# Performance work log

Measured on AMD Instinct MI355X. Metric: run time of the kernel, lower is better.

## Reference

```python
import jax, jax.numpy as jnp
import numpy as np

HIDDEN = 2048
N_HEADS = 16
N_KV_GROUPS = 4
HEAD_DIM = HIDDEN // N_HEADS  # 128
LATENT = 512
KV_SIZE = HIDDEN * N_KV_GROUPS // N_HEADS  # 512


def setup_inputs() -> dict:
    key = jax.random.key(0)
    ks = jax.random.split(key, 11)
    s = 0.02
    return {
        "hidden_states": jax.random.normal(ks[0], (2, 2048, HIDDEN), dtype=jnp.float32),
        "Wq": jax.random.normal(ks[1], (HIDDEN, HIDDEN), dtype=jnp.float32) * s,
        "bq": jnp.zeros((HIDDEN,), dtype=jnp.float32),
        "Wl": jax.random.normal(ks[2], (HIDDEN, LATENT), dtype=jnp.float32) * s,
        "bl": jnp.zeros((LATENT,), dtype=jnp.float32),
        "Wk": jax.random.normal(ks[3], (LATENT, KV_SIZE), dtype=jnp.float32) * s,
        "bk": jnp.zeros((KV_SIZE,), dtype=jnp.float32),
        "Wv": jax.random.normal(ks[4], (LATENT, KV_SIZE), dtype=jnp.float32) * s,
        "bv": jnp.zeros((KV_SIZE,), dtype=jnp.float32),
        "Wo": jax.random.normal(ks[5], (HIDDEN, HIDDEN), dtype=jnp.float32) * s,
        "bo": jnp.zeros((HIDDEN,), dtype=jnp.float32),
    }


def reference(hidden_states, Wq, bq, Wl, bl, Wk, bk, Wv, bv, Wo, bo):
    B, S, _ = hidden_states.shape
    heads_per_group = N_HEADS // N_KV_GROUPS

    q = hidden_states @ Wq + bq                      # [B,S,H*D]
    latent = hidden_states @ Wl + bl                 # [B,S,L]
    k = latent @ Wk + bk                             # [B,S,G*D]
    v = latent @ Wv + bv

    q = q.reshape(B, S, N_HEADS, HEAD_DIM).transpose(0, 2, 1, 3)        # [B,H,S,D]
    k = k.reshape(B, S, N_KV_GROUPS, HEAD_DIM).transpose(0, 2, 1, 3)    # [B,G,S,D]
    v = v.reshape(B, S, N_KV_GROUPS, HEAD_DIM).transpose(0, 2, 1, 3)

    # repeat_interleave over head dim: group g -> heads [g*hpg, (g+1)*hpg)
    k = jnp.repeat(k, heads_per_group, axis=1)       # [B,H,S,D]
    v = jnp.repeat(v, heads_per_group, axis=1)

    scale = 1.0 / np.sqrt(HEAD_DIM).astype(np.float32)
    scores = jnp.einsum("bhqd,bhkd->bhqk", q, k) * scale
    probs = jax.nn.softmax(scores, axis=-1)          # dropout p=0 (eval) -> identity
    ctx = jnp.einsum("bhqk,bhkd->bhqd", probs, v)    # [B,H,S,D]
    ctx = ctx.transpose(0, 2, 1, 3).reshape(B, S, HIDDEN)
    return ctx @ Wo + bo
```

## Files before the change

kernel.cpp:

```cpp
#include <hip/hip_runtime.h>
#include <stdint.h>


#define DEV static __device__ __forceinline__

using short8 = __attribute__((ext_vector_type(8))) short;
using f32x4  = __attribute__((ext_vector_type(4))) float;

typedef __attribute__((address_space(1))) void gvoid;
typedef __attribute__((address_space(3))) void lvoid;

DEV unsigned short f2b(float f) {
  unsigned u = __builtin_bit_cast(unsigned, f);
  unsigned r = (u + 0x7fffu + ((u >> 16) & 1u)) >> 16;
  return (unsigned short)r;
}
DEV float b2f(unsigned short s) {
  unsigned u = ((unsigned)s) << 16;
  return __builtin_bit_cast(float, u);
}

DEV unsigned cvtpk(float lo, float hi) {
  unsigned r;
  asm("v_cvt_pk_bf16_f32 %0, %1, %2" : "=v"(r) : "v"(lo), "v"(hi));
  return r;
}

DEV float ex2(float x) { return __builtin_amdgcn_exp2f(x); }

DEV void async16(const void* g, void* l) {
  __builtin_amdgcn_global_load_lds((gvoid*)(uintptr_t)g,
                                   (lvoid*)(uint32_t)(uintptr_t)l, 16, 0, 0);
}

DEV f32x4 mfma16(short8 a, short8 b, f32x4 c) {
  return __builtin_amdgcn_mfma_f32_16x16x32_bf16(a, b, c, 0, 0, 0);
}

__global__ __launch_bounds__(256) void mega_prep(
    const float* __restrict__ h, unsigned short* __restrict__ hb,
    const float* __restrict__ Wq, const float* __restrict__ Wl,
    const float* __restrict__ Wk, const float* __restrict__ Wv,
    const float* __restrict__ Wo,
    unsigned short* __restrict__ WqlT, unsigned short* __restrict__ WkvT,
    unsigned short* __restrict__ WoT,
    const float* __restrict__ bq, const float* __restrict__ bl,
    const float* __restrict__ bk, const float* __restrict__ bv,
    float* __restrict__ bql, float* __restrict__ bkv, float qscale) {
  __shared__ float tile[32][33];
  const int bid = blockIdx.x;
  const int tid = threadIdx.x;

  if (bid < 4096) {
    long i = ((long)bid * 256 + tid) * 8;
    float4 a = *(const float4*)(h + i);
    float4 b = *(const float4*)(h + i + 4);
    short8 o;
    o[0] = (short)f2b(a.x); o[1] = (short)f2b(a.y);
    o[2] = (short)f2b(a.z); o[3] = (short)f2b(a.w);
    o[4] = (short)f2b(b.x); o[5] = (short)f2b(b.y);
    o[6] = (short)f2b(b.z); o[7] = (short)f2b(b.w);
    *(short8*)(hb + i) = o;
    return;
  }

  const float* in; unsigned short* out; int R, C, bx, by; float sc = 1.0f;
  if (bid < 8192) {
    int l = bid - 4096; in = Wq; out = WqlT; R = 2048; C = 2048;
    bx = l & 63; by = l >> 6; sc = qscale;
  } else if (bid < 9216) {
    int l = bid - 8192; in = Wl; out = WqlT + 2048 * 2048; R = 2048; C = 512;
    bx = l & 15; by = l >> 4;
  } else if (bid < 9472) {
    int l = bid - 9216; in = Wk; out = WkvT; R = 512; C = 512;
    bx = l & 15; by = l >> 4;
  } else if (bid < 9728) {
    int l = bid - 9472; in = Wv; out = WkvT + 262144; R = 512; C = 512;
    bx = l & 15; by = l >> 4;
  } else if (bid < 13824) {
    int l = bid - 9728; in = Wo; out = WoT; R = 2048; C = 2048;
    bx = l & 63; by = l >> 6;
  } else {
    for (int t = tid; t < 2560; t += 256)
      bql[t] = (t < 2048) ? bq[t] * qscale : bl[t - 2048];
    for (int t = tid; t < 1024; t += 256)
      bkv[t] = (t < 512) ? bk[t] : bv[t - 512];
    return;
  }

  int bc = bx * 32, br = by * 32;
  int tx = tid & 31, ty0 = tid >> 5;
#pragma unroll
  for (int ty = ty0; ty < 32; ty += 8)
    tile[ty][tx] = in[(size_t)(br + ty) * C + bc + tx] * sc;
  __syncthreads();
#pragma unroll
  for (int ty = ty0; ty < 32; ty += 8)
    out[(size_t)(bc + ty) * R + br + tx] = f2b(tile[tx][ty]);
}

__global__ __launch_bounds__(256) void transpose_v(
    const unsigned short* __restrict__ in, unsigned short* __restrict__ out) {
  __shared__ float tile[32][33];
  int b = blockIdx.z;
  int bc = blockIdx.x * 32;
  int br = blockIdx.y * 32;
  const unsigned short* ip = in + (size_t)b * 2048 * 1024 + 512;
  unsigned short* op = out + (size_t)b * 512 * 2048;
  int tx = threadIdx.x & 31, ty0 = threadIdx.x >> 5;
#pragma unroll
  for (int ty = ty0; ty < 32; ty += 8)
    tile[ty][tx] = b2f(ip[(size_t)(br + ty) * 1024 + bc + tx]);
  __syncthreads();
#pragma unroll
  for (int ty = ty0; ty < 32; ty += 8)
    op[(size_t)(bc + ty) * 2048 + br + tx] = f2b(tile[tx][ty]);
}

template <int OUT_F32>
__global__ __launch_bounds__(256) void gemm_bt(
    const unsigned short* __restrict__ A, const unsigned short* __restrict__ Bt,
    const float* __restrict__ bias, void* __restrict__ Cout,
    int M, int N, int K, int lda, float scale) {
  __shared__ unsigned short As[128 * 32];
  __shared__ unsigned short Bs[128 * 32];
  int tid = threadIdx.x;
  int lane = tid & 63, wave = tid >> 6;
  int wr = wave >> 1, wc = wave & 1;
  int lq = lane & 15, grp = lane >> 4;
  int brow = blockIdx.y * 128, bcol = blockIdx.x * 128;

  f32x4 acc[4][4] = {};

  for (int k0 = 0; k0 < K; k0 += 32) {
    {
      int e0 = tid * 8;
      int r0 = e0 >> 5, c0 = e0 & 31;
      async16(A + (size_t)(brow + r0) * lda + k0 + c0, As + e0);
      async16(Bt + (size_t)(bcol + r0) * K + k0 + c0, Bs + e0);
      int e1 = (256 + tid) * 8;
      int r1 = e1 >> 5, c1 = e1 & 31;
      async16(A + (size_t)(brow + r1) * lda + k0 + c1, As + e1);
      async16(Bt + (size_t)(bcol + r1) * K + k0 + c1, Bs + e1);
    }
    __syncthreads();

    short8 af[4], bf[4];
#pragma unroll
    for (int m = 0; m < 4; m++)
      af[m] = *(const short8*)(As + (wr * 64 + m * 16 + lq) * 32 + grp * 8);
#pragma unroll
    for (int n = 0; n < 4; n++)
      bf[n] = *(const short8*)(Bs + (wc * 64 + n * 16 + lq) * 32 + grp * 8);
#pragma unroll
    for (int m = 0; m < 4; m++)
#pragma unroll
      for (int n = 0; n < 4; n++)
        acc[m][n] = mfma16(af[m], bf[n], acc[m][n]);
    __syncthreads();
  }

#pragma unroll
  for (int n = 0; n < 4; n++) {
    int col = bcol + wc * 64 + n * 16 + lq;
    float bv = bias[col];
#pragma unroll
    for (int m = 0; m < 4; m++) {
#pragma unroll
      for (int r = 0; r < 4; r++) {
        int row = brow + wr * 64 + m * 16 + grp * 4 + r;
        float v = (acc[m][n][r] + bv) * scale;
        if (OUT_F32)
          ((float*)Cout)[(size_t)row * N + col] = v;
        else
          ((unsigned short*)Cout)[(size_t)row * N + col] = f2b(v);
      }
    }
  }
}

template <int OUT_F32>
__global__ __launch_bounds__(512, 2) void gemm_bt_256(
    const unsigned short* __restrict__ A, const unsigned short* __restrict__ Bt,
    const float* __restrict__ bias, void* __restrict__ Cout,
    int M, int N, int K, float scale) {
  __shared__ __align__(1024) unsigned short As[2][16384];
  __shared__ __align__(1024) unsigned short Bs[2][8192];
  const int tid = threadIdx.x;
  const int lane = tid & 63, wave = tid >> 6;
  const int wr = wave >> 1, wc = wave & 1;
  const int lq = lane & 15, grp = lane >> 4;

  const int gx = gridDim.x;
  int nwg = gx * gridDim.y;
  int bid = blockIdx.y * gx + blockIdx.x;
  int wgid = (bid & 7) * (nwg >> 3) + (bid >> 3);
  int bx = wgid % gx, by = wgid / gx;
  const int brow = by * 256, bcol = bx * 128;

#define MKSLOT(db, mat, rb)                                            \
  ({ int d_ = (db) + lane * 16;                                        \
     int L_ = d_ ^ (((d_ >> 9) & 1) << 5);                             \
     (mat) + (size_t)((rb) + (L_ >> 7)) * K + ((L_ & 127) >> 1); })
  const int dbA0 = wave * 1024, dbA1 = dbA0 + 8192, dbA2 = dbA0 + 16384,
            dbA3 = dbA0 + 24576;
  const int dbB0 = (wave < 4) ? wave * 1024 : 8192 + (wave - 4) * 1024;
  const int dbB1 = dbB0 + 4096;
  const unsigned short* srcA0 = MKSLOT(dbA0, A, brow);
  const unsigned short* srcA1 = MKSLOT(dbA1, A, brow);
  const unsigned short* srcA2 = MKSLOT(dbA2, A, brow);
  const unsigned short* srcA3 = MKSLOT(dbA3, A, brow);
  const unsigned short* srcB0 = MKSLOT(dbB0, Bt, bcol);
  const unsigned short* srcB1 = MKSLOT(dbB1, Bt, bcol);
  char* dstA0 = (char*)&As[0][0] + dbA0 + lane * 16;
  char* dstA1 = (char*)&As[0][0] + dbA1 + lane * 16;
  char* dstA2 = (char*)&As[0][0] + dbA2 + lane * 16;
  char* dstA3 = (char*)&As[0][0] + dbA3 + lane * 16;
  char* dstB0 = (char*)&Bs[0][0] + dbB0 + lane * 16;
  char* dstB1 = (char*)&Bs[0][0] + dbB1 + lane * 16;
#define STA(i, b, k0) async16(srcA##i + (k0), dstA##i + (b) * 32768)
#define STB(i, b, k0) async16(srcB##i + (k0), dstB##i + (b) * 16384)

  auto ldA = [&](int cur, int row, int kk) -> short8 {
    int p = row * 128 + kk * 64 + grp * 16;
    p ^= ((p >> 9) & 1) << 5;
    return *(const short8*)((const char*)&As[cur][0] + p);
  };
  auto ldB = [&](int cur, int row, int kk) -> short8 {
    int p = row * 128 + kk * 64 + grp * 16;
    p ^= ((p >> 9) & 1) << 5;
    return *(const short8*)((const char*)&Bs[cur][0] + p);
  };

  f32x4 acc[4][4] = {};
  short8 af[4][2], bf[4][2];
  const int NT = K >> 6;

  STA(0, 0, 0); STA(1, 0, 0); STA(2, 0, 0); STA(3, 0, 0);
  STB(0, 0, 0); STB(1, 0, 0);
  asm volatile("s_waitcnt vmcnt(1)" ::: "memory");
  __builtin_amdgcn_s_barrier();

  for (int t = 0; t < NT; ++t) {
    const int cur = t & 1, nb = cur ^ 1;
    const bool pf = (t + 1 < NT);
    const int k0n = (t + 1) << 6;

#pragma unroll
    for (int m = 0; m < 4; m++) {
      af[m][0] = ldA(cur, wr * 64 + m * 16 + lq, 0);
      af[m][1] = ldA(cur, wr * 64 + m * 16 + lq, 1);
    }
#pragma unroll
    for (int n = 0; n < 2; n++) {
      bf[n][0] = ldB(cur, wc * 64 + n * 16 + lq, 0);
      bf[n][1] = ldB(cur, wc * 64 + n * 16 + lq, 1);
    }
    if (pf) { STA(0, nb, k0n); STA(1, nb, k0n); STA(2, nb, k0n); }
    __builtin_amdgcn_s_barrier();
    __builtin_amdgcn_s_setprio(1);
#pragma unroll
    for (int m = 0; m < 4; m++)
#pragma unroll
      for (int n = 0; n < 2; n++) {
        acc[m][n] = mfma16(af[m][0], bf[n][0], acc[m][n]);
        acc[m][n] = mfma16(af[m][1], bf[n][1], acc[m][n]);
      }
    __builtin_amdgcn_s_setprio(0);
    __builtin_amdgcn_s_barrier();

    if (pf) {
      STA(3, nb, k0n); STB(0, nb, k0n); STB(1, nb, k0n);
      asm volatile("s_waitcnt vmcnt(6)" ::: "memory");
    } else {
      asm volatile("s_waitcnt vmcnt(0)" ::: "memory");
    }
    __builtin_amdgcn_s_barrier();
#pragma unroll
    for (int n = 0; n < 2; n++) {
      bf[2 + n][0] = ldB(cur, wc * 64 + (2 + n) * 16 + lq, 0);
      bf[2 + n][1] = ldB(cur, wc * 64 + (2 + n) * 16 + lq, 1);
    }
    __builtin_amdgcn_s_setprio(1);
#pragma unroll
    for (int m = 0; m < 4; m++)
#pragma unroll
      for (int n = 2; n < 4; n++) {
        acc[m][n] = mfma16(af[m][0], bf[n][0], acc[m][n]);
        acc[m][n] = mfma16(af[m][1], bf[n][1], acc[m][n]);
      }
    __builtin_amdgcn_s_setprio(0);
    if (pf) {
      asm volatile("s_waitcnt vmcnt(1)" ::: "memory");
    }
    __builtin_amdgcn_s_barrier();
  }

#pragma unroll
  for (int n = 0; n < 4; n++) {
    int col = bcol + wc * 64 + n * 16 + lq;
    float bv = bias[col];
#pragma unroll
    for (int m = 0; m < 4; m++) {
#pragma unroll
      for (int r = 0; r < 4; r++) {
        int row = brow + wr * 64 + m * 16 + grp * 4 + r;
        float v = (acc[m][n][r] + bv) * scale;
        if (OUT_F32)
          ((float*)Cout)[(size_t)row * N + col] = v;
        else
          ((unsigned short*)Cout)[(size_t)row * N + col] = f2b(v);
      }
    }
  }
#undef STA
#undef STB
#undef MKSLOT
}

__global__ __launch_bounds__(256, 2) void attn_kernel(
    const unsigned short* __restrict__ q,
    const unsigned short* __restrict__ kv,
    const unsigned short* __restrict__ vt,
    unsigned short* __restrict__ ctx) {
  __shared__ unsigned short KV[2][32][512];
  const int lane = threadIdx.x & 63, wave = threadIdx.x >> 6;
  const int lq = lane & 15, grp = lane >> 4;
  const int bid = blockIdx.x;
  const int combo = bid & 7;
  const int slot = bid >> 3;
  const int b = combo >> 2, g = combo & 3;
  const int h = g * 4 + (slot >> 4);
  const int qbase = (slot & 15) * 128 + wave * 32;

  short8 qf[2][4];
#pragma unroll
  for (int qs = 0; qs < 2; qs++) {
    const unsigned short* qp =
        q + ((size_t)(b * 2048 + qbase + qs * 16 + lq)) * 2560 + h * 128 + grp * 8;
#pragma unroll
    for (int c = 0; c < 4; c++) qf[qs][c] = *(const short8*)(qp + c * 32);
  }

  f32x4 o[2][8] = {};
  float lsum[2] = {0.f, 0.f};
  const float C = 20.0f;

  const int kvperm = (lq >> 2) * 8 + (lq & 3);
  const unsigned short* kB = kv + (size_t)b * 2048 * 1024 + g * 128 + grp * 8;
  const unsigned short* vB =
      vt + ((size_t)((b * 4 + g) * 128 + lq)) * 2048 + grp * 8;
  const int fbase = wave * 8;
  unsigned short* dstb = &KV[0][fbase][0] + lane * 8;

  auto stage = [&](int bn, int kv0) {
    unsigned short* dst = dstb + bn * 16384;
    if (fbase < 16) {
#pragma unroll
      for (int j = 0; j < 8; j++) {
        int f = fbase + j, t = f >> 2, c = f & 3;
        const unsigned short* src =
            kB + (size_t)(kv0 + (t >> 1) * 32 + (t & 1) * 4 + kvperm) * 1024 + c * 32;
        async16(src, dst + j * 512);
      }
    } else {
#pragma unroll
      for (int j = 0; j < 8; j++) {
        int f = fbase - 16 + j, d0 = f >> 1, u = f & 1;
        const unsigned short* src = vB + (size_t)(d0 * 16) * 2048 + kv0 + u * 32;
        async16(src, dst + j * 512);
      }
    }
  };

  stage(0, 0);
  int buf = 0;
  for (int it = 0; it < 32; ++it) {
    __syncthreads();
    if (it < 31) stage(buf ^ 1, (it + 1) * 64);
    const unsigned short* Kb = &KV[buf][0][0] + lane * 8;

    f32x4 s[2][4] = {};
    __builtin_amdgcn_s_setprio(1);
#pragma unroll
    for (int c = 0; c < 4; c++) {
      short8 kf0 = *(const short8*)(Kb + (0 + c) * 512);
      short8 kf1 = *(const short8*)(Kb + (4 + c) * 512);
      short8 kf2 = *(const short8*)(Kb + (8 + c) * 512);
      short8 kf3 = *(const short8*)(Kb + (12 + c) * 512);
#pragma unroll
      for (int qs = 0; qs < 2; qs++) {
        s[qs][0] = mfma16(kf0, qf[qs][c], s[qs][0]);
        s[qs][1] = mfma16(kf1, qf[qs][c], s[qs][1]);
        s[qs][2] = mfma16(kf2, qf[qs][c], s[qs][2]);
        s[qs][3] = mfma16(kf3, qf[qs][c], s[qs][3]);
      }
    }
    __builtin_amdgcn_s_setprio(0);

    short8 pf[2][2];
#pragma unroll
    for (int qs = 0; qs < 2; qs++) {
      float ps = 0.f;
      union { short8 v; unsigned w[4]; } pk0, pk1;
#pragma unroll
      for (int t = 0; t < 4; t++) {
        float e0 = ex2(s[qs][t][0] - C);
        float e1 = ex2(s[qs][t][1] - C);
        float e2 = ex2(s[qs][t][2] - C);
        float e3 = ex2(s[qs][t][3] - C);
        ps += (e0 + e1) + (e2 + e3);
        unsigned w0 = cvtpk(e0, e1), w1 = cvtpk(e2, e3);
        if (t == 0) { pk0.w[0] = w0; pk0.w[1] = w1; }
        else if (t == 1) { pk0.w[2] = w0; pk0.w[3] = w1; }
        else if (t == 2) { pk1.w[0] = w0; pk1.w[1] = w1; }
        else { pk1.w[2] = w0; pk1.w[3] = w1; }
      }
      lsum[qs] += ps;
      pf[qs][0] = pk0.v;
      pf[qs][1] = pk1.v;
    }

    const unsigned short* Vb = Kb + 16 * 512;
    __builtin_amdgcn_s_setprio(1);
#pragma unroll
    for (int d0 = 0; d0 < 8; d0++) {
      short8 v0 = *(const short8*)(Vb + (d0 * 2 + 0) * 512);
      short8 v1 = *(const short8*)(Vb + (d0 * 2 + 1) * 512);
#pragma unroll
      for (int qs = 0; qs < 2; qs++) {
        o[qs][d0] = mfma16(pf[qs][0], v0, o[qs][d0]);
        o[qs][d0] = mfma16(pf[qs][1], v1, o[qs][d0]);
      }
    }
    __builtin_amdgcn_s_setprio(0);
    buf ^= 1;
  }

  unsigned short* cp = ctx + ((size_t)(b * 2048 + qbase)) * 2048 + h * 128;
#pragma unroll
  for (int qs = 0; qs < 2; qs++) {
    float l = lsum[qs];
    l += __shfl_xor(l, 16);
    l += __shfl_xor(l, 32);
    float ri = 1.0f / l;
    float r0 = __shfl(ri, grp * 4 + 0), r1 = __shfl(ri, grp * 4 + 1);
    float r2 = __shfl(ri, grp * 4 + 2), r3 = __shfl(ri, grp * 4 + 3);
#pragma unroll
    for (int d0 = 0; d0 < 8; d0++) {
      int col = d0 * 16 + lq;
      cp[(size_t)(qs * 16 + grp * 4 + 0) * 2048 + col] = f2b(o[qs][d0][0] * r0);
      cp[(size_t)(qs * 16 + grp * 4 + 1) * 2048 + col] = f2b(o[qs][d0][1] * r1);
      cp[(size_t)(qs * 16 + grp * 4 + 2) * 2048 + col] = f2b(o[qs][d0][2] * r2);
      cp[(size_t)(qs * 16 + grp * 4 + 3) * 2048 + col] = f2b(o[qs][d0][3] * r3);
    }
  }
}

extern "C" void kernel_launch(void* const* d_in, const int* in_sizes, int n_in,
                              void* d_out, int out_size, void* d_ws, size_t ws_size,
                              hipStream_t stream) {
  const float* h  = (const float*)d_in[0];
  const float* Wq = (const float*)d_in[1];
  const float* bq = (const float*)d_in[2];
  const float* Wl = (const float*)d_in[3];
  const float* bl = (const float*)d_in[4];
  const float* Wk = (const float*)d_in[5];
  const float* bk = (const float*)d_in[6];
  const float* Wv = (const float*)d_in[7];
  const float* bv = (const float*)d_in[8];
  const float* Wo = (const float*)d_in[9];
  const float* bo = (const float*)d_in[10];
  float* out = (float*)d_out;

  const int M = 4096;

  char* w = (char*)d_ws;
  auto take = [&](size_t elems) {
    void* p = (void*)w;
    w += (elems * 2 + 255) & ~(size_t)255;
    return (unsigned short*)p;
  };
  unsigned short* hb   = take(8388608);
  unsigned short* WqlT = take(5242880);
  unsigned short* WkvT = take(524288);
  unsigned short* WoT  = take(4194304);
  unsigned short* qlat = take(10485760);
  unsigned short* kvb  = take(4194304);
  unsigned short* vtb  = take(2097152);
  unsigned short* ctx  = take(8388608);
  float* bql = (float*)take(2560);
  float* bkv = (float*)take(1024);

  const float scale = 0.08838834764831845f * 1.4426950408889634f;

  mega_prep<<<13825, 256, 0, stream>>>(h, hb, Wq, Wl, Wk, Wv, Wo,
                                       WqlT, WkvT, WoT,
                                       bq, bl, bk, bv, bql, bkv, scale);

  gemm_bt_256<0><<<dim3(20, 16), 512, 0, stream>>>(hb, WqlT, bql, qlat, M, 2560, 2048, 1.0f);
  gemm_bt<0><<<dim3(8, 32), 256, 0, stream>>>(qlat + 2048, WkvT, bkv, kvb, M, 1024, 512, 2560, 1.0f);

  transpose_v<<<dim3(16, 64, 2), 256, 0, stream>>>(kvb, vtb);

  attn_kernel<<<512, 256, 0, stream>>>(qlat, kvb, vtb, ctx);

  gemm_bt_256<1><<<dim3(16, 16), 512, 0, stream>>>(ctx, WoT, bo, out, M, 2048, 2048, 1.0f);
}
```

Baseline: 244.2 us.

## Replace 256x128 GEMM with 256x256 tile four-phase pipelined kernel

```diff
diff --git a/kernel.cpp b/kernel.cpp
--- a/kernel.cpp
+++ b/kernel.cpp
@@ -180,142 +180,163 @@
 }
 
 template <int OUT_F32>
-__global__ __launch_bounds__(512, 2) void gemm_bt_256(
+__global__ __launch_bounds__(512, 1) void gemm_8ph(
     const unsigned short* __restrict__ A, const unsigned short* __restrict__ Bt,
     const float* __restrict__ bias, void* __restrict__ Cout,
     int M, int N, int K, float scale) {
-  __shared__ __align__(1024) unsigned short As[2][16384];
-  __shared__ __align__(1024) unsigned short Bs[2][8192];
-  const int tid = threadIdx.x;
-  const int lane = tid & 63, wave = tid >> 6;
-  const int wr = wave >> 1, wc = wave & 1;
+  __shared__ __align__(1024) unsigned short L[2][32768];
+  const int tid = threadIdx.x, lane = tid & 63, wave = tid >> 6;
   const int lq = lane & 15, grp = lane >> 4;
+  const int wr = wave >> 2, wc = wave & 3;
 
   const int gx = gridDim.x;
   int nwg = gx * gridDim.y;
   int bid = blockIdx.y * gx + blockIdx.x;
   int wgid = (bid & 7) * (nwg >> 3) + (bid >> 3);
   int bx = wgid % gx, by = wgid / gx;
-  const int brow = by * 256, bcol = bx * 128;
-
-#define MKSLOT(db, mat, rb)                                            \
-  ({ int d_ = (db) + lane * 16;                                        \
-     int L_ = d_ ^ (((d_ >> 9) & 1) << 5);                             \
-     (mat) + (size_t)((rb) + (L_ >> 7)) * K + ((L_ & 127) >> 1); })
-  const int dbA0 = wave * 1024, dbA1 = dbA0 + 8192, dbA2 = dbA0 + 16384,
-            dbA3 = dbA0 + 24576;
-  const int dbB0 = (wave < 4) ? wave * 1024 : 8192 + (wave - 4) * 1024;
-  const int dbB1 = dbB0 + 4096;
-  const unsigned short* srcA0 = MKSLOT(dbA0, A, brow);
-  const unsigned short* srcA1 = MKSLOT(dbA1, A, brow);
-  const unsigned short* srcA2 = MKSLOT(dbA2, A, brow);
-  const unsigned short* srcA3 = MKSLOT(dbA3, A, brow);
-  const unsigned short* srcB0 = MKSLOT(dbB0, Bt, bcol);
-  const unsigned short* srcB1 = MKSLOT(dbB1, Bt, bcol);
-  char* dstA0 = (char*)&As[0][0] + dbA0 + lane * 16;
-  char* dstA1 = (char*)&As[0][0] + dbA1 + lane * 16;
-  char* dstA2 = (char*)&As[0][0] + dbA2 + lane * 16;
-  char* dstA3 = (char*)&As[0][0] + dbA3 + lane * 16;
-  char* dstB0 = (char*)&Bs[0][0] + dbB0 + lane * 16;
-  char* dstB1 = (char*)&Bs[0][0] + dbB1 + lane * 16;
-#define STA(i, b, k0) async16(srcA##i + (k0), dstA##i + (b) * 32768)
-#define STB(i, b, k0) async16(srcB##i + (k0), dstB##i + (b) * 16384)
-
-  auto ldA = [&](int cur, int row, int kk) -> short8 {
-    int p = row * 128 + kk * 64 + grp * 16;
-    p ^= ((p >> 9) & 1) << 5;
-    return *(const short8*)((const char*)&As[cur][0] + p);
+  const int brow = by * 256, bcol = bx * 256;
+
+  const unsigned short* srcA[2];
+  const unsigned short* srcB[2];
+  unsigned short* dstA[2];
+  unsigned short* dstB[2];
+#pragma unroll
+  for (int j = 0; j < 2; j++) {
+    int f = wave + j * 8, kk = f & 1, fi = f >> 1;
+    int awr = fi >> 2, aml = fi & 3;
+    srcA[j] = A + (size_t)(brow + (awr * 8 + aml) * 16 + lq) * K + kk * 32 + grp * 8;
+    dstA[j] = &L[0][0] + f * 512 + lane * 8;
+    int bwc = fi >> 1, bnl = fi & 1;
+    srcB[j] = Bt + (size_t)(bcol + (bwc * 4 + bnl) * 16 + lq) * K + kk * 32 + grp * 8;
+    dstB[j] = &L[0][0] + 16384 + f * 512 + lane * 8;
+  }
+  auto stgA = [&](int p, int mh, int k0) {
+#pragma unroll
+    for (int j = 0; j < 2; j++)
+      async16(srcA[j] + (size_t)mh * 64 * K + k0, dstA[j] + p * 32768 + mh * 8192);
   };
-  auto ldB = [&](int cur, int row, int kk) -> short8 {
-    int p = row * 128 + kk * 64 + grp * 16;
-    p ^= ((p >> 9) & 1) << 5;
-    return *(const short8*)((const char*)&Bs[cur][0] + p);
+  auto stgB = [&](int p, int nh, int k0) {
+#pragma unroll
+    for (int j = 0; j < 2; j++)
+      async16(srcB[j] + (size_t)nh * 32 * K + k0, dstB[j] + p * 32768 + nh * 8192);
   };
-
-  f32x4 acc[4][4] = {};
-  short8 af[4][2], bf[4][2];
+  auto ldAf = [&](int p, int mh, int ml, int kk) -> short8 {
+    return *(const short8*)(&L[0][0] + p * 32768 + mh * 8192 +
+                            ((wr * 4 + ml) * 2 + kk) * 512 + lane * 8);
+  };
+  auto ldBf = [&](int p, int nh, int nl, int kk) -> short8 {
+    return *(const short8*)(&L[0][0] + p * 32768 + 16384 + nh * 8192 +
+                            ((wc * 2 + nl) * 2 + kk) * 512 + lane * 8);
+  };
+
+  f32x4 acc[8][4] = {};
+  short8 af[4][2], bf0[2][2], bf1[2][2];
   const int NT = K >> 6;
 
-  STA(0, 0, 0); STA(1, 0, 0); STA(2, 0, 0); STA(3, 0, 0);
-  STB(0, 0, 0); STB(1, 0, 0);
-  asm volatile("s_waitcnt vmcnt(1)" ::: "memory");
+  stgA(0, 0, 0); stgB(0, 0, 0); stgB(0, 1, 0); stgA(0, 1, 0);
+  asm volatile("s_waitcnt vmcnt(4)" ::: "memory");
   __builtin_amdgcn_s_barrier();
 
-  for (int t = 0; t < NT; ++t) {
-    const int cur = t & 1, nb = cur ^ 1;
-    const bool pf = (t + 1 < NT);
-    const int k0n = (t + 1) << 6;
-
-#pragma unroll
-    for (int m = 0; m < 4; m++) {
-      af[m][0] = ldA(cur, wr * 64 + m * 16 + lq, 0);
-      af[m][1] = ldA(cur, wr * 64 + m * 16 + lq, 1);
-    }
-#pragma unroll
-    for (int n = 0; n < 2; n++) {
-      bf[n][0] = ldB(cur, wc * 64 + n * 16 + lq, 0);
-      bf[n][1] = ldB(cur, wc * 64 + n * 16 + lq, 1);
-    }
-    if (pf) { STA(0, nb, k0n); STA(1, nb, k0n); STA(2, nb, k0n); }
+  for (int T = 0; T < NT; ++T) {
+    const int cur = T & 1, nxt = cur ^ 1;
+    const bool pf = (T + 1 < NT);
+    const int k1 = (T + 1) << 6;
+
+#pragma unroll
+    for (int ml = 0; ml < 4; ml++) {
+      af[ml][0] = ldAf(cur, 0, ml, 0);
+      af[ml][1] = ldAf(cur, 0, ml, 1);
+    }
+#pragma unroll
+    for (int nl = 0; nl < 2; nl++) {
+      bf0[nl][0] = ldBf(cur, 0, nl, 0);
+      bf0[nl][1] = ldBf(cur, 0, nl, 1);
+    }
+    if (pf) stgA(nxt, 0, k1);
+    __builtin_amdgcn_s_setprio(1);
+#pragma unroll
+    for (int ml = 0; ml < 4; ml++)
+#pragma unroll
+      for (int nl = 0; nl < 2; nl++) {
+        acc[ml][nl] = mfma16(af[ml][0], bf0[nl][0], acc[ml][nl]);
+        acc[ml][nl] = mfma16(af[ml][1], bf0[nl][1], acc[ml][nl]);
+      }
+    __builtin_amdgcn_s_setprio(0);
+    if (pf) asm volatile("s_waitcnt vmcnt(4)" ::: "memory");
+    else    asm volatile("s_waitcnt vmcnt(2)" ::: "memory");
     __builtin_amdgcn_s_barrier();
+
+#pragma unroll
+    for (int nl = 0; nl < 2; nl++) {
+      bf1[nl][0] = ldBf(cur, 1, nl, 0);
+      bf1[nl][1] = ldBf(cur, 1, nl, 1);
+    }
+    if (pf) stgB(nxt, 0, k1);
     __builtin_amdgcn_s_setprio(1);
 #pragma unroll
-    for (int m = 0; m < 4; m++)
-#pragma unroll
-      for (int n = 0; n < 2; n++) {
-        acc[m][n] = mfma16(af[m][0], bf[n][0], acc[m][n]);
-        acc[m][n] = mfma16(af[m][1], bf[n][1], acc[m][n]);
+    for (int ml = 0; ml < 4; ml++)
+#pragma unroll
+      for (int nl = 0; nl < 2; nl++) {
+        acc[ml][2 + nl] = mfma16(af[ml][0], bf1[nl][0], acc[ml][2 + nl]);
+        acc[ml][2 + nl] = mfma16(af[ml][1], bf1[nl][1], acc[ml][2 + nl]);
+      }
+    __builtin_amdgcn_s_setprio(0);
+    if (pf) asm volatile("s_waitcnt vmcnt(4)" ::: "memory");
+    else    asm volatile("s_waitcnt vmcnt(0)" ::: "memory");
+    __builtin_amdgcn_s_barrier();
+
+#pragma unroll
+    for (int ml = 0; ml < 4; ml++) {
+      af[ml][0] = ldAf(cur, 1, ml, 0);
+      af[ml][1] = ldAf(cur, 1, ml, 1);
+    }
+    if (pf) stgB(nxt, 1, k1);
+    __builtin_amdgcn_s_setprio(1);
+#pragma unroll
+    for (int ml = 0; ml < 4; ml++)
+#pragma unroll
+      for (int nl = 0; nl < 2; nl++) {
+        acc[4 + ml][nl] = mfma16(af[ml][0], bf0[nl][0], acc[4 + ml][nl]);
+        acc[4 + ml][nl] = mfma16(af[ml][1], bf0[nl][1], acc[4 + ml][nl]);
       }
     __builtin_amdgcn_s_setprio(0);
     __builtin_amdgcn_s_barrier();
 
-    if (pf) {
-      STA(3, nb, k0n); STB(0, nb, k0n); STB(1, nb, k0n);
-      asm volatile("s_waitcnt vmcnt(6)" ::: "memory");
-    } else {
-      asm volatile("s_waitcnt vmcnt(0)" ::: "memory");
-    }
+    if (pf) stgA(nxt, 1, k1);
+    __builtin_amdgcn_s_setprio(1);
+#pragma unroll
+    for (int ml = 0; ml < 4; ml++)
+#pragma unroll
+      for (int nl = 0; nl < 2; nl++) {
+        acc[4 + ml][2 + nl] = mfma16(af[ml][0], bf1[nl][0], acc[4 + ml][2 + nl]);
+        acc[4 + ml][2 + nl] = mfma16(af[ml][1], bf1[nl][1], acc[4 + ml][2 + nl]);
+      }
+    __builtin_amdgcn_s_setprio(0);
+    if (pf) asm volatile("s_waitcnt vmcnt(4)" ::: "memory");
     __builtin_amdgcn_s_barrier();
-#pragma unroll
-    for (int n = 0; n < 2; n++) {
-      bf[2 + n][0] = ldB(cur, wc * 64 + (2 + n) * 16 + lq, 0);
-      bf[2 + n][1] = ldB(cur, wc * 64 + (2 + n) * 16 + lq, 1);
-    }
-    __builtin_amdgcn_s_setprio(1);
-#pragma unroll
-    for (int m = 0; m < 4; m++)
-#pragma unroll
-      for (int n = 2; n < 4; n++) {
-        acc[m][n] = mfma16(af[m][0], bf[n][0], acc[m][n]);
-        acc[m][n] = mfma16(af[m][1], bf[n][1], acc[m][n]);
-      }
-    __builtin_amdgcn_s_setprio(0);
-    if (pf) {
-      asm volatile("s_waitcnt vmcnt(1)" ::: "memory");
-    }
-    __builtin_amdgcn_s_barrier();
-  }
-
-#pragma unroll
-  for (int n = 0; n < 4; n++) {
-    int col = bcol + wc * 64 + n * 16 + lq;
-    float bv = bias[col];
-#pragma unroll
-    for (int m = 0; m < 4; m++) {
-#pragma unroll
-      for (int r = 0; r < 4; r++) {
-        int row = brow + wr * 64 + m * 16 + grp * 4 + r;
-        float v = (acc[m][n][r] + bv) * scale;
-        if (OUT_F32)
-          ((float*)Cout)[(size_t)row * N + col] = v;
-        else
-          ((unsigned short*)Cout)[(size_t)row * N + col] = f2b(v);
-      }
-    }
-  }
-#undef STA
-#undef STB
-#undef MKSLOT
+  }
+
+#pragma unroll
+  for (int mh = 0; mh < 2; mh++)
+#pragma unroll
+    for (int ml = 0; ml < 4; ml++)
+#pragma unroll
+      for (int nh = 0; nh < 2; nh++)
+#pragma unroll
+        for (int nl = 0; nl < 2; nl++) {
+          int col = bcol + wc * 64 + (nh * 2 + nl) * 16 + lq;
+          float bv = bias[col];
+          f32x4 a = acc[mh * 4 + ml][nh * 2 + nl];
+#pragma unroll
+          for (int r = 0; r < 4; r++) {
+            int row = brow + wr * 128 + (mh * 4 + ml) * 16 + grp * 4 + r;
+            float v = (a[r] + bv) * scale;
+            if (OUT_F32)
+              ((float*)Cout)[(size_t)row * N + col] = v;
+            else
+              ((unsigned short*)Cout)[(size_t)row * N + col] = f2b(v);
+          }
+        }
 }
 
 __global__ __launch_bounds__(256, 2) void attn_kernel(
@@ -498,12 +519,12 @@
                                        WqlT, WkvT, WoT,
                                        bq, bl, bk, bv, bql, bkv, scale);
 
-  gemm_bt_256<0><<<dim3(20, 16), 512, 0, stream>>>(hb, WqlT, bql, qlat, M, 2560, 2048, 1.0f);
+  gemm_8ph<0><<<dim3(10, 16), 512, 0, stream>>>(hb, WqlT, bql, qlat, M, 2560, 2048, 1.0f);
   gemm_bt<0><<<dim3(8, 32), 256, 0, stream>>>(qlat + 2048, WkvT, bkv, kvb, M, 1024, 512, 2560, 1.0f);
 
   transpose_v<<<dim3(16, 64, 2), 256, 0, stream>>>(kvb, vtb);
 
   attn_kernel<<<512, 256, 0, stream>>>(qlat, kvb, vtb, ctx);
 
-  gemm_bt_256<1><<<dim3(16, 16), 512, 0, stream>>>(ctx, WoT, bo, out, M, 2048, 2048, 1.0f);
-}
+  gemm_8ph<1><<<dim3(8, 16), 512, 0, stream>>>(ctx, WoT, bo, out, M, 2048, 2048, 1.0f);
+}
```

Result: no change. 241.5 us (median of 2 runs) (-1.1%).
